# Kernel optimization log

Hardware: AMD Instinct MI355X
Metric: run time of the kernel (lower is better)

Reference implementation:

```python
import jax, jax.numpy as jnp
import numpy as np

B = 32        # graphs per batch
MAXN = 2048   # max nodes per graph (dense batch length)
HEADS = 8
DH = 64       # head dim (512/8)
M = 256       # FAVOR+ random features
D = 512
EPS = 1e-5    # batchnorm eps
KEPS = 1e-6   # performer stabilizer


def _batchnorm(x, g, b):
    # torch BatchNorm1d training-mode: biased batch statistics over node dim
    mu = jnp.mean(x, axis=0)
    var = jnp.mean((x - mu) ** 2, axis=0)
    return (x - mu) * jax.lax.rsqrt(var + EPS) * g + b


def setup_inputs() -> dict:
    key = jax.random.key(0)
    ks = jax.random.split(key, 10)
    sizes = 1024 + (np.arange(B) * 131) % 1025   # ragged graph sizes in [1024, 2048]
    N = int(sizes.sum())                          # 48544
    E = N * 8
    batch = jnp.asarray(np.repeat(np.arange(B), sizes), dtype=jnp.int32)
    edge_index = jax.random.randint(ks[0], (2, E), 0, N, dtype=jnp.int32)
    s = 1.0 / np.sqrt(D)
    return {
        'x': jax.random.normal(ks[1], (N, D), jnp.float32),
        'batch': batch,
        'edge_index': edge_index,
        'norm1_g': jnp.ones((D,), jnp.float32),
        'norm1_b': jnp.zeros((D,), jnp.float32),
        'norm2_g': jnp.ones((D,), jnp.float32),
        'norm2_b': jnp.zeros((D,), jnp.float32),
        'W_conv': jax.random.normal(ks[2], (D, D), jnp.float32) * s,
        'b_conv': jnp.zeros((D,), jnp.float32),
        'Wq': jax.random.normal(ks[3], (D, D), jnp.float32) * s,
        'Wk': jax.random.normal(ks[4], (D, D), jnp.float32) * s,
        'Wv': jax.random.normal(ks[5], (D, D), jnp.float32) * s,
        'Wo': jax.random.normal(ks[6], (D, D), jnp.float32) * s,
        'proj': jax.random.normal(ks[7], (M, DH), jnp.float32),
    }


def _forward(x, batch, edge_index, norm1_g, norm1_b, norm2_g, norm2_b,
             W_conv, b_conv, Wq, Wk, Wv, Wo, proj):
    N = x.shape[0]
    E = edge_index.shape[1]
    h = x

    # norm1 (+ dropout p=0 -> identity) then local GNN conv (mean-agg GCN + linear + relu)
    xn = _batchnorm(x, norm1_g, norm1_b)
    msg = xn[edge_index[0]]                                        # [E, D] gather
    agg = jax.ops.segment_sum(msg, edge_index[1], num_segments=N)  # [N, D] scatter-add
    deg = jax.ops.segment_sum(jnp.ones((E,), x.dtype), edge_index[1], num_segments=N)
    agg = agg / jnp.maximum(deg, 1.0)[:, None]
    conv_out = jax.nn.relu(agg @ W_conv + b_conv)

    # to_dense_batch(h, batch) -> h_dense [B, MAXN, D], mask [B, MAXN]
    counts = jax.ops.segment_sum(jnp.ones((N,), jnp.int32), batch, num_segments=B)
    offsets = jnp.concatenate([jnp.zeros((1,), jnp.int32), jnp.cumsum(counts)[:-1]])
    pos = jnp.arange(N, dtype=jnp.int32) - offsets[batch]
    h_dense = jnp.zeros((B, MAXN, D), x.dtype).at[batch, pos].set(h)
    mask = jnp.zeros((B, MAXN), bool).at[batch, pos].set(True)

    # Performer FAVOR+ non-causal self-attention
    def heads(t, W):
        return (t @ W).reshape(B, MAXN, HEADS, DH).transpose(0, 2, 1, 3)  # [B,H,MAXN,DH]
    q, k, v = heads(h_dense, Wq), heads(h_dense, Wk), heads(h_dense, Wv)

    scale = DH ** -0.25  # data normalizer applied to q and k each

    def phi(t, is_query):
        t = t * scale
        u = jnp.einsum('bhnd,md->bhnm', t, proj)           # [B,H,MAXN,M]
        diag = 0.5 * jnp.sum(t * t, axis=-1, keepdims=True)
        if is_query:
            m_ = jnp.max(u, axis=-1, keepdims=True)
        else:
            m_ = jnp.max(u, axis=(-2, -1), keepdims=True)
        return jnp.exp(u - diag - jax.lax.stop_gradient(m_)) / np.sqrt(M) + KEPS

    qf = phi(q, True)
    kf = phi(k, False) * mask[:, None, :, None]   # zero padded keys
    vm = v * mask[:, None, :, None]

    kv = jnp.einsum('bhnm,bhnd->bhmd', kf, vm)                    # [B,H,M,DH]
    z = 1.0 / (jnp.einsum('bhnm,bhm->bhn', qf, kf.sum(axis=2)) + KEPS)
    attn = jnp.einsum('bhnm,bhmd->bhnd', qf, kv) * z[..., None]   # [B,H,MAXN,DH]
    attn = attn.transpose(0, 2, 1, 3).reshape(B, MAXN, D) @ Wo

    h_attn = attn[batch, pos]                                      # gather back: [mask]

    return _batchnorm(conv_out + h_attn + h, norm2_g, norm2_b)


def reference(x, batch, edge_index, norm1_g, norm1_b, norm2_g, norm2_b,
              W_conv, b_conv, Wq, Wk, Wv, Wo, proj):
    return _forward(x, batch, edge_index, norm1_g, norm1_b, norm2_g, norm2_b,
                    W_conv, b_conv, Wq, Wk, Wv, Wo, proj)
```

## Files before the change

kernel.cpp:

```cpp
#include <hip/hip_runtime.h>
#include <stdint.h>

#define CDIV(a,b) (((a)+(b)-1)/(b))

typedef __attribute__((ext_vector_type(4))) float f32x4;
typedef __attribute__((ext_vector_type(8))) short s16x8;
typedef __attribute__((ext_vector_type(8))) unsigned short u16x8;
typedef __attribute__((ext_vector_type(4))) unsigned short u16x4;

__device__ __forceinline__ float bf2f(unsigned short u) {
  union { unsigned int i; float f; } c; c.i = ((unsigned int)u) << 16; return c.f;
}
__device__ __forceinline__ unsigned short f2bf(float f) {
  union { float f; unsigned int i; } c; c.f = f;
  unsigned int u = c.i;
  u += 0x7fffu + ((u >> 16) & 1u);
  return (unsigned short)(u >> 16);
}

template<int BM, int BN, int WM, int WN, int EPI>
__global__ __launch_bounds__(256) void gemm_bt(
    const unsigned short* __restrict__ A, const unsigned short* __restrict__ B,
    void* __restrict__ Cout, const float* __restrict__ aux,
    int K, int lda, int ldb, int ldc, long zsC, int Mstore)
{
  constexpr int MT = BM / (WM * 16);
  constexpr int NT = BN / (WN * 16);
  constexpr int LDT = 40;
  __shared__ unsigned short As[BM * LDT];
  __shared__ unsigned short Bs[BN * LDT];
  const int tid = threadIdx.x, wid = tid >> 6, lane = tid & 63;
  const int wr = wid / WN, wc = wid % WN;
  long m0 = (long)blockIdx.y * BM;
  const int n0 = blockIdx.x * BN;
  f32x4 acc[MT][NT] = {};
  for (int k0 = 0; k0 < K; k0 += 32) {
    #pragma unroll
    for (int c = tid; c < BM * 4; c += 256) {
      int row = c >> 2, c8 = (c & 3) * 8;
      *(u16x8*)(&As[row * LDT + c8]) = *(const u16x8*)(A + (m0 + row) * lda + k0 + c8);
    }
    #pragma unroll
    for (int c = tid; c < BN * 4; c += 256) {
      int row = c >> 2, c8 = (c & 3) * 8;
      *(u16x8*)(&Bs[row * LDT + c8]) = *(const u16x8*)(B + (long)(n0 + row) * ldb + k0 + c8);
    }
    __syncthreads();
    s16x8 af[MT], bfv[NT];
    #pragma unroll
    for (int mt = 0; mt < MT; mt++)
      af[mt] = *(const s16x8*)(&As[(wr * MT * 16 + mt * 16 + (lane & 15)) * LDT + ((lane >> 4) * 8)]);
    #pragma unroll
    for (int nt = 0; nt < NT; nt++)
      bfv[nt] = *(const s16x8*)(&Bs[(wc * NT * 16 + nt * 16 + (lane & 15)) * LDT + ((lane >> 4) * 8)]);
    #pragma unroll
    for (int mt = 0; mt < MT; mt++)
      #pragma unroll
      for (int nt = 0; nt < NT; nt++)
        acc[mt][nt] = __builtin_amdgcn_mfma_f32_16x16x32_bf16(af[mt], bfv[nt], acc[mt][nt], 0, 0, 0);
    __syncthreads();
  }
  #pragma unroll
  for (int mt = 0; mt < MT; mt++) {
    const int rl0 = wr * (MT * 16) + mt * 16 + ((lane >> 4) << 2);
    #pragma unroll
    for (int nt = 0; nt < NT; nt++) {
      const int col = n0 + wc * (NT * 16) + nt * 16 + (lane & 15);
      #pragma unroll
      for (int i = 0; i < 4; i++) {
        long r = m0 + rl0 + i;
        if (r < Mstore) {
          float v = acc[mt][nt][i];
          long ci = r * ldc + col;
          if constexpr (EPI == 5) {
            float o = v + aux[col];
            o = o > 0.f ? o : 0.f;
            ((float*)Cout)[ci] += o;
          } else if constexpr (EPI == 7) {
            ((unsigned short*)Cout)[(long)(col >> 6) * zsC + r * 64 + (col & 63)] = f2bf(v);
          } else if constexpr (EPI == 8) {
            ((float*)Cout)[ci] = v + aux[ci];
          }
        }
      }
    }
  }
}

__global__ __launch_bounds__(256) void k_kmax(
    const unsigned short* __restrict__ kvqh, const unsigned short* __restrict__ projb,
    const unsigned int* __restrict__ offs, unsigned int* __restrict__ kmax, long Npad) {
  __shared__ float wmax[4];
  const int tid = threadIdx.x, wid = tid >> 6, lane = tid & 63;
  const int b = blockIdx.y, h = blockIdx.z;
  const unsigned int off = offs[b];
  const int nb = (int)(offs[b + 1] - off);
  const int m0 = blockIdx.x * 64;
  if (m0 >= nb) return;
  const unsigned short* A = kvqh + ((long)(8 + h) * Npad + off + m0) * 64;
  f32x4 acc[4][4] = {};
  #pragma unroll
  for (int k0 = 0; k0 < 64; k0 += 32) {
    s16x8 af[4], bfv[4];
    #pragma unroll
    for (int mt = 0; mt < 4; mt++)
      af[mt] = *(const s16x8*)(A + (long)(mt * 16 + (lane & 15)) * 64 + k0 + ((lane >> 4) * 8));
    #pragma unroll
    for (int nt = 0; nt < 4; nt++)
      bfv[nt] = *(const s16x8*)(projb + (long)(wid * 64 + nt * 16 + (lane & 15)) * 64 + k0 + ((lane >> 4) * 8));
    #pragma unroll
    for (int mt = 0; mt < 4; mt++)
      #pragma unroll
      for (int nt = 0; nt < 4; nt++)
        acc[mt][nt] = __builtin_amdgcn_mfma_f32_16x16x32_bf16(af[mt], bfv[nt], acc[mt][nt], 0, 0, 0);
  }
  float bm = -3.0e38f;
  #pragma unroll
  for (int mt = 0; mt < 4; mt++)
    #pragma unroll
    for (int i = 0; i < 4; i++) {
      int row = mt * 16 + ((lane >> 4) << 2) + i;
      if (m0 + row < nb) {
        #pragma unroll
        for (int nt = 0; nt < 4; nt++) bm = fmaxf(bm, acc[mt][nt][i]);
      }
    }
  #pragma unroll
  for (int s = 1; s < 64; s <<= 1) bm = fmaxf(bm, __shfl_xor(bm, s));
  if (lane == 0) wmax[wid] = bm;
  __syncthreads();
  if (tid == 0) {
    float m = fmaxf(fmaxf(wmax[0], wmax[1]), fmaxf(wmax[2], wmax[3]));
    atomicMax(&kmax[b * 8 + h], __float_as_uint(fmaxf(m, 0.f)));
  }
}

__global__ __launch_bounds__(256) void k_kvm(
    const unsigned short* __restrict__ kvqh, const unsigned short* __restrict__ projb,
    const unsigned int* __restrict__ offs, const unsigned int* __restrict__ kmax,
    unsigned short* __restrict__ kvTb, float* __restrict__ kfsum, long Npad) {
  constexpr int TLD = 72;
  __shared__ unsigned short vsT[2][64 * TLD];
  __shared__ unsigned short kfsT[64 * TLD];
  const int tid = threadIdx.x, wid = tid >> 6, lane = tid & 63;
  const int mblk = blockIdx.x, b = blockIdx.y, h = blockIdx.z;
  const unsigned int off = offs[b];
  const int nb = (int)(offs[b + 1] - off);
  const float km = __uint_as_float(kmax[b * 8 + h]);
  const unsigned short* Kp = kvqh + ((long)(8 + h) * Npad + off) * 64;
  const unsigned short* Vp = kvqh + ((long)(16 + h) * Npad + off) * 64;
  const unsigned short* Pp = projb + (long)(mblk * 64 + wid * 16) * 64;
  const int l15 = lane & 15, hi = lane >> 4;
  const int mloc = wid * 16 + l15;

  #pragma unroll
  for (int c = tid; c < 512; c += 256) {
    int row = c >> 3, c8 = (c & 7) * 8;
    int rot = (c & 7) * 8;
    u16x8 v = *(const u16x8*)(Vp + (long)row * 64 + c8);
    #pragma unroll
    for (int j = 0; j < 8; j++) vsT[0][(c8 + j) * TLD + ((row + rot) & 63)] = v[j];
  }
  __syncthreads();

  f32x4 akv[4] = {};
  float ksum = 0.f;
  int buf = 0;
  for (int n0 = 0; n0 < nb; n0 += 64) {
    f32x4 acc[4] = {};
    float dsum[4] = {0.f, 0.f, 0.f, 0.f};
    #pragma unroll
    for (int k0 = 0; k0 < 64; k0 += 32) {
      s16x8 af[4];
      #pragma unroll
      for (int mt = 0; mt < 4; mt++)
        af[mt] = *(const s16x8*)(Kp + ((long)n0 + mt * 16 + l15) * 64 + k0 + hi * 8);
      s16x8 bfv = *(const s16x8*)(Pp + (long)l15 * 64 + k0 + hi * 8);
      #pragma unroll
      for (int mt = 0; mt < 4; mt++) {
        #pragma unroll
        for (int j = 0; j < 8; j++) {
          float a = bf2f((unsigned short)af[mt][j]);
          dsum[mt] += a * a;
        }
        acc[mt] = __builtin_amdgcn_mfma_f32_16x16x32_bf16(af[mt], bfv, acc[mt], 0, 0, 0);
      }
    }
    float rs[4];
    #pragma unroll
    for (int mt = 0; mt < 4; mt++) {
      float s = dsum[mt];
      s += __shfl_xor(s, 16); s += __shfl_xor(s, 32);
      rs[mt] = 0.0625f * s;
    }
    #pragma unroll
    for (int mt = 0; mt < 4; mt++) {
      int r0 = mt * 16 + hi * 4;
      float e[4];
      #pragma unroll
      for (int i = 0; i < 4; i++) {
        float dg = __shfl(rs[mt], hi * 4 + i);
        e[i] = (n0 + r0 + i < nb) ? (__expf(acc[mt][i] - dg - km) * 0.0625f + 1e-6f) : 0.f;
      }
      ksum += e[0] + e[1] + e[2] + e[3];
      unsigned int p0 = (unsigned int)f2bf(e[0]) | ((unsigned int)f2bf(e[1]) << 16);
      unsigned int p1 = (unsigned int)f2bf(e[2]) | ((unsigned int)f2bf(e[3]) << 16);
      *(unsigned int*)(&kfsT[mloc * TLD + r0]) = p0;
      *(unsigned int*)(&kfsT[mloc * TLD + r0 + 2]) = p1;
    }
    if (n0 + 64 < nb) {
      #pragma unroll
      for (int c = tid; c < 512; c += 256) {
        int row = c >> 3, c8 = (c & 7) * 8;
        int rot = (c & 7) * 8;
        u16x8 v = *(const u16x8*)(Vp + ((long)n0 + 64 + row) * 64 + c8);
        #pragma unroll
        for (int j = 0; j < 8; j++) vsT[buf ^ 1][(c8 + j) * TLD + ((row + rot) & 63)] = v[j];
      }
    }
    #pragma unroll
    for (int ks = 0; ks < 2; ks++) {
      s16x8 bB = *(const s16x8*)(&kfsT[mloc * TLD + ks * 32 + hi * 8]);
      #pragma unroll
      for (int mt2 = 0; mt2 < 4; mt2++) {
        int d = mt2 * 16 + l15;
        int rrot = ((ks * 32 + hi * 8) + ((d >> 3) & 7) * 8) & 63;
        s16x8 aA = *(const s16x8*)(&vsT[buf][d * TLD + rrot]);
        akv[mt2] = __builtin_amdgcn_mfma_f32_16x16x32_bf16(aA, bB, akv[mt2], 0, 0, 0);
      }
    }
    __syncthreads();
    buf ^= 1;
  }
  long base = ((long)b * 8 + h) * 16384;
  const int m = mblk * 64 + mloc;
  #pragma unroll
  for (int mt2 = 0; mt2 < 4; mt2++)
    #pragma unroll
    for (int i = 0; i < 4; i++) {
      int d = mt2 * 16 + hi * 4 + i;
      kvTb[base + (long)d * 256 + m] = f2bf(akv[mt2][i]);
    }
  ksum += __shfl_xor(ksum, 16); ksum += __shfl_xor(ksum, 32);
  if (hi == 0) kfsum[((long)b * 8 + h) * 256 + m] = ksum;
}

__global__ __launch_bounds__(256) void k_qflash(
    const unsigned short* __restrict__ qh_all, const unsigned short* __restrict__ projb,
    const unsigned short* __restrict__ kvTb, const float* __restrict__ kfsum,
    const unsigned int* __restrict__ offs, unsigned short* __restrict__ attn, long Npad) {
  constexpr int QLDT = 264;
  __shared__ unsigned short qfs[64 * QLDT];
  __shared__ float skf[256];
  __shared__ float sdiag[64];
  __shared__ float smax[4][64];
  __shared__ float szp[4][64];
  const int tid = threadIdx.x, wid = tid >> 6, lane = tid & 63;
  const int b = blockIdx.y, h = blockIdx.z;
  const unsigned int off = offs[b];
  const int nb = (int)(offs[b + 1] - off);
  const int m0 = blockIdx.x * 64;
  if (m0 >= nb) return;
  const unsigned short* A = qh_all + ((long)h * Npad + off + m0) * 64;
  skf[tid] = kfsum[((long)b * 8 + h) * 256 + tid];
  f32x4 acc[4][4] = {};
  float dsum[4] = {0.f, 0.f, 0.f, 0.f};
  #pragma unroll
  for (int k0 = 0; k0 < 64; k0 += 32) {
    s16x8 af[4], bfv[4];
    #pragma unroll
    for (int mt = 0; mt < 4; mt++)
      af[mt] = *(const s16x8*)(A + (long)(mt * 16 + (lane & 15)) * 64 + k0 + ((lane >> 4) * 8));
    #pragma unroll
    for (int nt = 0; nt < 4; nt++)
      bfv[nt] = *(const s16x8*)(projb + (long)(wid * 64 + nt * 16 + (lane & 15)) * 64 + k0 + ((lane >> 4) * 8));
    if (wid == 0) {
      #pragma unroll
      for (int mt = 0; mt < 4; mt++)
        #pragma unroll
        for (int j = 0; j < 8; j++) {
          float a = bf2f((unsigned short)af[mt][j]);
          dsum[mt] += a * a;
        }
    }
    #pragma unroll
    for (int mt = 0; mt < 4; mt++)
      #pragma unroll
      for (int nt = 0; nt < 4; nt++)
        acc[mt][nt] = __builtin_amdgcn_mfma_f32_16x16x32_bf16(af[mt], bfv[nt], acc[mt][nt], 0, 0, 0);
  }
  if (wid == 0) {
    #pragma unroll
    for (int mt = 0; mt < 4; mt++) {
      float s = dsum[mt];
      s += __shfl_xor(s, 16); s += __shfl_xor(s, 32);
      if (lane < 16) sdiag[mt * 16 + lane] = 0.0625f * s;
    }
  }
  #pragma unroll
  for (int mt = 0; mt < 4; mt++)
    #pragma unroll
    for (int i = 0; i < 4; i++) {
      float rm = fmaxf(fmaxf(acc[mt][0][i], acc[mt][1][i]), fmaxf(acc[mt][2][i], acc[mt][3][i]));
      rm = fmaxf(rm, __shfl_xor(rm, 1)); rm = fmaxf(rm, __shfl_xor(rm, 2));
      rm = fmaxf(rm, __shfl_xor(rm, 4)); rm = fmaxf(rm, __shfl_xor(rm, 8));
      if ((lane & 15) == 0) smax[wid][mt * 16 + ((lane >> 4) << 2) + i] = rm;
    }
  __syncthreads();
  #pragma unroll
  for (int mt = 0; mt < 4; mt++)
    #pragma unroll
    for (int i = 0; i < 4; i++) {
      int row = mt * 16 + ((lane >> 4) << 2) + i;
      float rm = fmaxf(fmaxf(smax[0][row], smax[1][row]), fmaxf(smax[2][row], smax[3][row]));
      float dg = sdiag[row];
      float zp = 0.f;
      #pragma unroll
      for (int nt = 0; nt < 4; nt++) {
        int col = wid * 64 + nt * 16 + (lane & 15);
        float e = __expf(acc[mt][nt][i] - dg - rm) * 0.0625f + 1e-6f;
        qfs[row * QLDT + col] = f2bf(e);
        zp += e * skf[col];
      }
      zp += __shfl_xor(zp, 1); zp += __shfl_xor(zp, 2);
      zp += __shfl_xor(zp, 4); zp += __shfl_xor(zp, 8);
      if ((lane & 15) == 0) szp[wid][row] = zp;
    }
  __syncthreads();
  const unsigned short* kvb = kvTb + ((long)b * 8 + h) * 16384;
  f32x4 acc2[4] = {};
  #pragma unroll
  for (int ks = 0; ks < 8; ks++) {
    s16x8 aq = *(const s16x8*)(&qfs[(wid * 16 + (lane & 15)) * QLDT + ks * 32 + ((lane >> 4) * 8)]);
    #pragma unroll
    for (int ntd = 0; ntd < 4; ntd++) {
      s16x8 bk = *(const s16x8*)(kvb + (long)(ntd * 16 + (lane & 15)) * 256 + ks * 32 + ((lane >> 4) * 8));
      acc2[ntd] = __builtin_amdgcn_mfma_f32_16x16x32_bf16(aq, bk, acc2[ntd], 0, 0, 0);
    }
  }
  #pragma unroll
  for (int ntd = 0; ntd < 4; ntd++)
    #pragma unroll
    for (int i = 0; i < 4; i++) {
      int row = wid * 16 + ((lane >> 4) << 2) + i;
      if (m0 + row < nb) {
        float zr = 1.f / (szp[0][row] + szp[1][row] + szp[2][row] + szp[3][row] + 1e-6f);
        attn[(long)(off + m0 + row) * 512 + h * 64 + ntd * 16 + (lane & 15)] = f2bf(acc2[ntd][i] * zr);
      }
    }
}


__global__ void k_fill(float* __restrict__ out, long n, float v) {
  long i = (long)blockIdx.x * 256 + threadIdx.x;
  if (i < n) out[i] = v;
}

__global__ void k_convert_x(const float* __restrict__ x, unsigned short* __restrict__ xb,
                            long ntotal, long nreal) {
  long i = ((long)blockIdx.x * 256 + threadIdx.x) * 4;
  if (i >= ntotal) return;
  u16x4 o;
  if (i < nreal) {
    f32x4 v = *(const f32x4*)(x + i);
    o[0] = f2bf(v[0]); o[1] = f2bf(v[1]); o[2] = f2bf(v[2]); o[3] = f2bf(v[3]);
  } else { o[0] = 0; o[1] = 0; o[2] = 0; o[3] = 0; }
  *(u16x4*)(xb + i) = o;
}

__global__ void k_transall(const float* __restrict__ w0, const float* __restrict__ w1,
                           const float* __restrict__ w2, const float* __restrict__ w3,
                           const float* __restrict__ w4, unsigned short* __restrict__ out) {
  long idx = (long)blockIdx.x * 256 + threadIdx.x;
  if (idx >= (5L << 18)) return;
  int which = (int)(idx >> 18);
  int r = (int)(idx & 262143);
  int n = r >> 9, k = r & 511;
  const float* w = which == 0 ? w0 : which == 1 ? w1 : which == 2 ? w2 : which == 3 ? w3 : w4;
  out[idx] = f2bf(w[k * 512 + n]);
}

__global__ void k_scale_copy_bf(const float* __restrict__ in, unsigned short* __restrict__ out,
                                int n, float scl) {
  int i = blockIdx.x * 256 + threadIdx.x;
  if (i < n) out[i] = f2bf(in[i] * scl);
}

__global__ void k_bn_stats(const float* __restrict__ x, float* __restrict__ s1,
                           float* __restrict__ s2, int N, int rpb) {
  int t = threadIdx.x;
  int r0 = blockIdx.x * rpb;
  int r1 = min(N, r0 + rpb);
  float a1 = 0, a2 = 0, b1 = 0, b2 = 0;
  for (int r = r0; r < r1; r++) {
    float va = x[(long)r * 512 + t];
    float vb = x[(long)r * 512 + t + 256];
    a1 += va; a2 += va * va; b1 += vb; b2 += vb * vb;
  }
  atomicAdd(&s1[t], a1); atomicAdd(&s2[t], a2);
  atomicAdd(&s1[t + 256], b1); atomicAdd(&s2[t + 256], b2);
}

__global__ void k_bn_final(const float* __restrict__ s1, const float* __restrict__ s2,
                           const float* __restrict__ g, const float* __restrict__ b,
                           float* __restrict__ a, float* __restrict__ c, float invN) {
  int t = threadIdx.x;
  float mu = s1[t] * invN;
  float var = s2[t] * invN - mu * mu;
  float inv = rsqrtf(var + 1e-5f);
  float av = g[t] * inv;
  a[t] = av;
  c[t] = b[t] - mu * av;
}

__global__ void k_deg(const int* __restrict__ ed, unsigned int* __restrict__ deg, long E) {
  long i = (long)blockIdx.x * 256 + threadIdx.x;
  if (i < E) atomicAdd(&deg[ed[i]], 1u);
}

__global__ void k_offs(const int* __restrict__ batch, unsigned int* __restrict__ offs, int N) {
  int i = blockIdx.x * 256 + threadIdx.x;
  if (i >= N) return;
  int b = batch[i];
  if (i == 0) { for (int bb = 0; bb <= b; bb++) offs[bb] = 0; }
  else {
    int pb = batch[i - 1];
    if (pb != b) for (int bb = pb + 1; bb <= b; bb++) offs[bb] = i;
  }
  if (i == N - 1) { for (int bb = b + 1; bb <= 32; bb++) offs[bb] = N; }
}

__global__ __launch_bounds__(1024) void k_scan_nodes(const unsigned int* __restrict__ deg,
                                                     unsigned int* __restrict__ rowstart, int N) {
  __shared__ unsigned int wsum[16];
  __shared__ unsigned int carry_s;
  int t = threadIdx.x, lane = t & 63, wid = t >> 6;
  if (t == 0) carry_s = 0;
  __syncthreads();
  for (int base = 0; base < N; base += 1024) {
    int i = base + t;
    unsigned int v = (i < N) ? deg[i] : 0;
    unsigned int sc = v;
    #pragma unroll
    for (int s = 1; s < 64; s <<= 1) {
      unsigned int u = __shfl_up(sc, s);
      if (lane >= s) sc += u;
    }
    if (lane == 63) wsum[wid] = sc;
    __syncthreads();
    unsigned int woff = 0, tot = 0;
    #pragma unroll
    for (int w = 0; w < 16; w++) { unsigned int s = wsum[w]; if (w < wid) woff += s; tot += s; }
    unsigned int carry = carry_s;
    if (i < N) rowstart[i] = carry + woff + sc - v;
    __syncthreads();
    if (t == 0) carry_s = carry + tot;
    __syncthreads();
  }
  if (threadIdx.x == 0) rowstart[N] = carry_s;
}

__global__ void k_csr_fill(const int* __restrict__ es, const int* __restrict__ ed,
                           const unsigned int* __restrict__ rowstart,
                           unsigned int* __restrict__ cursor, int* __restrict__ csr, long E) {
  long e = (long)blockIdx.x * 256 + threadIdx.x;
  if (e >= E) return;
  int d = ed[e];
  unsigned int slot = atomicAdd(&cursor[d], 1u);
  csr[rowstart[d] + slot] = es[e];
}

__global__ __launch_bounds__(128) void k_gather(const int* __restrict__ csr,
                                                const unsigned int* __restrict__ rowstart,
                                                const float* __restrict__ x,
                                                const float* __restrict__ a1, const float* __restrict__ c1,
                                                unsigned short* __restrict__ conv_in, int N) {
  long n = blockIdx.x;
  int c = threadIdx.x * 4;
  u16x4 o; o[0] = 0; o[1] = 0; o[2] = 0; o[3] = 0;
  if (n < N) {
    unsigned int r0 = rowstart[n], r1 = rowstart[n + 1];
    if (r1 > r0) {
      f32x4 acc0 = {}, acc1 = {};
      unsigned int j = r0;
      for (; j + 2 <= r1; j += 2) {
        int s0 = csr[j], s1 = csr[j + 1];
        acc0 += *(const f32x4*)(x + (long)s0 * 512 + c);
        acc1 += *(const f32x4*)(x + (long)s1 * 512 + c);
      }
      if (j < r1) { int s0 = csr[j]; acc0 += *(const f32x4*)(x + (long)s0 * 512 + c); }
      f32x4 acc = acc0 + acc1;
      float inv = 1.f / (float)(r1 - r0);
      o[0] = f2bf(acc[0] * inv * a1[c + 0] + c1[c + 0]);
      o[1] = f2bf(acc[1] * inv * a1[c + 1] + c1[c + 1]);
      o[2] = f2bf(acc[2] * inv * a1[c + 2] + c1[c + 2]);
      o[3] = f2bf(acc[3] * inv * a1[c + 3] + c1[c + 3]);
    }
  }
  *(u16x4*)(conv_in + n * 512 + c) = o;
}

__global__ void k_stats(const float* __restrict__ y, float* __restrict__ s1,
                        float* __restrict__ s2, int N, int rpb) {
  int t = threadIdx.x;
  int r0 = blockIdx.x * rpb;
  int r1 = min(N, r0 + rpb);
  float a1 = 0, a2 = 0, b1 = 0, b2 = 0;
  for (int r = r0; r < r1; r++) {
    float va = y[(long)r * 512 + t];
    float vb = y[(long)r * 512 + t + 256];
    a1 += va; a2 += va * va; b1 += vb; b2 += vb * vb;
  }
  atomicAdd(&s1[t], a1); atomicAdd(&s2[t], a2);
  atomicAdd(&s1[t + 256], b1); atomicAdd(&s2[t + 256], b2);
}

__global__ void k_bn_apply(float* __restrict__ y, const float* __restrict__ a,
                           const float* __restrict__ c, long total) {
  long i4 = ((long)blockIdx.x * 256 + threadIdx.x) * 4;
  if (i4 >= total) return;
  int col = (int)(i4 & 511);
  f32x4 v = *(const f32x4*)(y + i4);
  #pragma unroll
  for (int j = 0; j < 4; j++) v[j] = v[j] * a[col + j] + c[col + j];
  *(f32x4*)(y + i4) = v;
}


extern "C" void kernel_launch(void* const* d_in, const int* in_sizes, int n_in,
                              void* d_out, int out_size, void* d_ws, size_t ws_size,
                              hipStream_t stream) {
  (void)n_in; (void)out_size;
  const float* x = (const float*)d_in[0];
  const int* batch = (const int*)d_in[1];
  const int* eidx = (const int*)d_in[2];
  const float* n1g = (const float*)d_in[3];
  const float* n1b = (const float*)d_in[4];
  const float* n2g = (const float*)d_in[5];
  const float* n2b = (const float*)d_in[6];
  const float* wconv = (const float*)d_in[7];
  const float* bconv = (const float*)d_in[8];
  const float* wq = (const float*)d_in[9];
  const float* wk = (const float*)d_in[10];
  const float* wv = (const float*)d_in[11];
  const float* wo = (const float*)d_in[12];
  const float* proj = (const float*)d_in[13];

  const int N = in_sizes[1];
  const long E = in_sizes[2] / 2;
  const long Npad = CDIV(N, 128) * 128 + 256;
  const int Mb = (int)((CDIV(N, 128) * 128 + 128) / 128);
  const int* es = eidx;
  const int* ed = eidx + E;
  float* out = (float*)d_out;

  char* p = (char*)d_ws;
  auto alloc = [&](size_t bytes) -> char* {
    char* r = p;
    p += (bytes + 255) & ~(size_t)255;
    return r;
  };
  unsigned short* kvqh = (unsigned short*)alloc((size_t)24 * Npad * 64 * 2);
  unsigned short* xbf  = (unsigned short*)alloc((size_t)Npad * 512 * 2);
  unsigned short* kvT_b = (unsigned short*)alloc((size_t)32 * 8 * 16384 * 2);
  unsigned short* wts   = (unsigned short*)alloc((size_t)5 * 512 * 512 * 2);
  unsigned short* proj_s = (unsigned short*)alloc((size_t)256 * 64 * 2);
  float* bn1_acc = (float*)alloc(1024 * 4);
  float* bn1_ac  = (float*)alloc(1024 * 4);
  float* bn2_acc = (float*)alloc(1024 * 4);
  float* bn2_ac  = (float*)alloc(1024 * 4);
  unsigned int* deg      = (unsigned int*)alloc((size_t)N * 4);
  unsigned int* offs     = (unsigned int*)alloc(33 * 4);
  unsigned int* kmax     = (unsigned int*)alloc(32 * 8 * 4);
  float* kfsum = (float*)alloc((size_t)32 * 8 * 256 * 4);
  unsigned int* rowstart = (unsigned int*)alloc((size_t)(N + 1) * 4);
  unsigned int* cursor   = (unsigned int*)alloc((size_t)N * 4);
  int* csr               = (int*)alloc((size_t)E * 4);
  size_t required = (size_t)(p - (char*)d_ws);
  if (required > ws_size) {
    k_fill<<<(int)CDIV((long)N * 512, 256), 256, 0, stream>>>(
        out, (long)N * 512, 1.0e6f + (float)(ws_size >> 20));
    return;
  }
  unsigned short* wqkv_t  = wts;
  unsigned short* wconv_t = wts + 3 * 512 * 512;
  unsigned short* wo_t    = wts + 4 * 512 * 512;
  unsigned short* attn_all = xbf;
  unsigned short* conv_in  = xbf;

  hipMemsetAsync(deg, 0, (size_t)N * 4, stream);
  hipMemsetAsync(cursor, 0, (size_t)N * 4, stream);
  hipMemsetAsync(kmax, 0, 32 * 8 * 4, stream);
  hipMemsetAsync(bn1_acc, 0, 1024 * 4, stream);
  hipMemsetAsync(bn2_acc, 0, 1024 * 4, stream);

  k_convert_x<<<(int)CDIV(Npad * 512 / 4, 256), 256, 0, stream>>>(x, xbf, Npad * 512, (long)N * 512);
  k_transall<<<(int)CDIV(5L << 18, 256), 256, 0, stream>>>(wq, wk, wv, wconv, wo, wts);
  k_scale_copy_bf<<<CDIV(256 * 64, 256), 256, 0, stream>>>(proj, proj_s, 256 * 64, 0.35355339059327373f);

  int rpb = CDIV(N, 1024);
  k_bn_stats<<<1024, 256, 0, stream>>>(x, bn1_acc, bn1_acc + 512, N, rpb);
  k_bn_final<<<1, 512, 0, stream>>>(bn1_acc, bn1_acc + 512, n1g, n1b, bn1_ac, bn1_ac + 512, 1.f / N);
  k_deg<<<(int)CDIV(E, 256), 256, 0, stream>>>(ed, deg, E);
  k_offs<<<CDIV(N, 256), 256, 0, stream>>>(batch, offs, N);
  k_scan_nodes<<<1, 1024, 0, stream>>>(deg, rowstart, N);
  k_csr_fill<<<(int)CDIV(E, 256), 256, 0, stream>>>(es, ed, rowstart, cursor, csr, E);

  gemm_bt<128, 128, 2, 2, 7><<<dim3(12, Mb), 256, 0, stream>>>(
      xbf, wqkv_t, kvqh, nullptr, 512, 512, 512, 0, (long)Npad * 64, (int)Npad);

  k_kmax<<<dim3(32, 32, 8), 256, 0, stream>>>(kvqh, proj_s, offs, kmax, Npad);
  k_kvm<<<dim3(4, 32, 8), 256, 0, stream>>>(kvqh, proj_s, offs, kmax, kvT_b, kfsum, Npad);

  k_qflash<<<dim3(32, 32, 8), 256, 0, stream>>>(
      kvqh, proj_s, kvT_b, kfsum, offs, attn_all, Npad);

  gemm_bt<128, 128, 2, 2, 8><<<dim3(4, Mb), 256, 0, stream>>>(
      attn_all, wo_t, out, x, 512, 512, 512, 512, 0, N);

  k_gather<<<(int)(CDIV(N, 128) * 128), 128, 0, stream>>>(csr, rowstart, x, bn1_ac, bn1_ac + 512, conv_in, N);
  gemm_bt<128, 128, 2, 2, 5><<<dim3(4, Mb), 256, 0, stream>>>(
      conv_in, wconv_t, out, bconv, 512, 512, 512, 512, 0, N);

  k_stats<<<1024, 256, 0, stream>>>(out, bn2_acc, bn2_acc + 512, N, rpb);
  k_bn_final<<<1, 512, 0, stream>>>(bn2_acc, bn2_acc + 512, n2g, n2b, bn2_ac, bn2_ac + 512, 1.f / N);
  k_bn_apply<<<(int)CDIV((long)N * 512 / 4, 256), 256, 0, stream>>>(out, bn2_ac, bn2_ac + 512, (long)N * 512);
}
```

Before: 1.187 ms.

## Restructure query feature kernel per-wave and fold normalizer into kv matmul

```diff
diff --git a/kernel.cpp b/kernel.cpp
--- a/kernel.cpp
+++ b/kernel.cpp
@@ -17,6 +17,8 @@
   u += 0x7fffu + ((u >> 16) & 1u);
   return (unsigned short)(u >> 16);
 }
+
+#define KVROWS 80
 
 template<int BM, int BN, int WM, int WN, int EPI>
 __global__ __launch_bounds__(256) void gemm_bt(
@@ -138,7 +140,7 @@
 __global__ __launch_bounds__(256) void k_kvm(
     const unsigned short* __restrict__ kvqh, const unsigned short* __restrict__ projb,
     const unsigned int* __restrict__ offs, const unsigned int* __restrict__ kmax,
-    unsigned short* __restrict__ kvTb, float* __restrict__ kfsum, long Npad) {
+    unsigned short* __restrict__ kvTb, long Npad) {
   constexpr int TLD = 72;
   __shared__ unsigned short vsT[2][64 * TLD];
   __shared__ unsigned short kfsT[64 * TLD];
@@ -232,7 +234,7 @@
     __syncthreads();
     buf ^= 1;
   }
-  long base = ((long)b * 8 + h) * 16384;
+  long base = ((long)b * 8 + h) * (KVROWS * 256);
   const int m = mblk * 64 + mloc;
   #pragma unroll
   for (int mt2 = 0; mt2 < 4; mt2++)
@@ -242,112 +244,82 @@
       kvTb[base + (long)d * 256 + m] = f2bf(akv[mt2][i]);
     }
   ksum += __shfl_xor(ksum, 16); ksum += __shfl_xor(ksum, 32);
-  if (hi == 0) kfsum[((long)b * 8 + h) * 256 + m] = ksum;
-}
-
-__global__ __launch_bounds__(256) void k_qflash(
+  if (hi == 0) kvTb[base + 64 * 256 + m] = f2bf(ksum);
+}
+
+__global__ __launch_bounds__(256, 4) void k_qflash(
     const unsigned short* __restrict__ qh_all, const unsigned short* __restrict__ projb,
-    const unsigned short* __restrict__ kvTb, const float* __restrict__ kfsum,
-    const unsigned int* __restrict__ offs, unsigned short* __restrict__ attn, long Npad) {
+    const unsigned short* __restrict__ kvTb, const unsigned int* __restrict__ offs,
+    unsigned short* __restrict__ attn, long Npad) {
   constexpr int QLDT = 264;
-  __shared__ unsigned short qfs[64 * QLDT];
-  __shared__ float skf[256];
-  __shared__ float sdiag[64];
-  __shared__ float smax[4][64];
-  __shared__ float szp[4][64];
+  __shared__ unsigned short qfs[4][16 * QLDT];
   const int tid = threadIdx.x, wid = tid >> 6, lane = tid & 63;
+  const int l15 = lane & 15, hi = lane >> 4;
   const int b = blockIdx.y, h = blockIdx.z;
   const unsigned int off = offs[b];
   const int nb = (int)(offs[b + 1] - off);
-  const int m0 = blockIdx.x * 64;
+  const int m0 = blockIdx.x * 64 + wid * 16;
   if (m0 >= nb) return;
-  const unsigned short* A = qh_all + ((long)h * Npad + off + m0) * 64;
-  skf[tid] = kfsum[((long)b * 8 + h) * 256 + tid];
-  f32x4 acc[4][4] = {};
-  float dsum[4] = {0.f, 0.f, 0.f, 0.f};
+  const unsigned short* Q = qh_all + ((long)h * Npad + off + m0) * 64;
+
+  f32x4 acc[16] = {};
+  float dsq = 0.f;
   #pragma unroll
   for (int k0 = 0; k0 < 64; k0 += 32) {
-    s16x8 af[4], bfv[4];
-    #pragma unroll
-    for (int mt = 0; mt < 4; mt++)
-      af[mt] = *(const s16x8*)(A + (long)(mt * 16 + (lane & 15)) * 64 + k0 + ((lane >> 4) * 8));
-    #pragma unroll
-    for (int nt = 0; nt < 4; nt++)
-      bfv[nt] = *(const s16x8*)(projb + (long)(wid * 64 + nt * 16 + (lane & 15)) * 64 + k0 + ((lane >> 4) * 8));
-    if (wid == 0) {
-      #pragma unroll
-      for (int mt = 0; mt < 4; mt++)
-        #pragma unroll
-        for (int j = 0; j < 8; j++) {
-          float a = bf2f((unsigned short)af[mt][j]);
-          dsum[mt] += a * a;
-        }
-    }
-    #pragma unroll
-    for (int mt = 0; mt < 4; mt++)
-      #pragma unroll
-      for (int nt = 0; nt < 4; nt++)
-        acc[mt][nt] = __builtin_amdgcn_mfma_f32_16x16x32_bf16(af[mt], bfv[nt], acc[mt][nt], 0, 0, 0);
-  }
-  if (wid == 0) {
-    #pragma unroll
-    for (int mt = 0; mt < 4; mt++) {
-      float s = dsum[mt];
-      s += __shfl_xor(s, 16); s += __shfl_xor(s, 32);
-      if (lane < 16) sdiag[mt * 16 + lane] = 0.0625f * s;
-    }
-  }
-  #pragma unroll
-  for (int mt = 0; mt < 4; mt++)
-    #pragma unroll
-    for (int i = 0; i < 4; i++) {
-      float rm = fmaxf(fmaxf(acc[mt][0][i], acc[mt][1][i]), fmaxf(acc[mt][2][i], acc[mt][3][i]));
-      rm = fmaxf(rm, __shfl_xor(rm, 1)); rm = fmaxf(rm, __shfl_xor(rm, 2));
-      rm = fmaxf(rm, __shfl_xor(rm, 4)); rm = fmaxf(rm, __shfl_xor(rm, 8));
-      if ((lane & 15) == 0) smax[wid][mt * 16 + ((lane >> 4) << 2) + i] = rm;
-    }
-  __syncthreads();
-  #pragma unroll
-  for (int mt = 0; mt < 4; mt++)
-    #pragma unroll
-    for (int i = 0; i < 4; i++) {
-      int row = mt * 16 + ((lane >> 4) << 2) + i;
-      float rm = fmaxf(fmaxf(smax[0][row], smax[1][row]), fmaxf(smax[2][row], smax[3][row]));
-      float dg = sdiag[row];
-      float zp = 0.f;
-      #pragma unroll
-      for (int nt = 0; nt < 4; nt++) {
-        int col = wid * 64 + nt * 16 + (lane & 15);
-        float e = __expf(acc[mt][nt][i] - dg - rm) * 0.0625f + 1e-6f;
-        qfs[row * QLDT + col] = f2bf(e);
-        zp += e * skf[col];
-      }
-      zp += __shfl_xor(zp, 1); zp += __shfl_xor(zp, 2);
-      zp += __shfl_xor(zp, 4); zp += __shfl_xor(zp, 8);
-      if ((lane & 15) == 0) szp[wid][row] = zp;
-    }
-  __syncthreads();
-  const unsigned short* kvb = kvTb + ((long)b * 8 + h) * 16384;
-  f32x4 acc2[4] = {};
+    s16x8 bfv = *(const s16x8*)(Q + (long)l15 * 64 + k0 + hi * 8);
+    #pragma unroll
+    for (int j = 0; j < 8; j++) {
+      float qv = bf2f((unsigned short)bfv[j]);
+      dsq += qv * qv;
+    }
+    #pragma unroll
+    for (int mt = 0; mt < 16; mt++) {
+      s16x8 af = *(const s16x8*)(projb + (long)(mt * 16 + l15) * 64 + k0 + hi * 8);
+      acc[mt] = __builtin_amdgcn_mfma_f32_16x16x32_bf16(af, bfv, acc[mt], 0, 0, 0);
+    }
+  }
+  dsq += __shfl_xor(dsq, 16); dsq += __shfl_xor(dsq, 32);
+  float rm = -3.0e38f;
+  #pragma unroll
+  for (int mt = 0; mt < 16; mt++)
+    #pragma unroll
+    for (int i = 0; i < 4; i++) rm = fmaxf(rm, acc[mt][i]);
+  rm = fmaxf(rm, __shfl_xor(rm, 16)); rm = fmaxf(rm, __shfl_xor(rm, 32));
+  const float sub = 0.0625f * dsq + rm;
+
+  unsigned short* myq = &qfs[wid][0];
+  #pragma unroll
+  for (int mt = 0; mt < 16; mt++) {
+    u16x4 o;
+    #pragma unroll
+    for (int i = 0; i < 4; i++)
+      o[i] = f2bf(__expf(acc[mt][i] - sub) * 0.0625f + 1e-6f);
+    *(u16x4*)(&myq[l15 * QLDT + mt * 16 + hi * 4]) = o;
+  }
+
+  const unsigned short* kvb = kvTb + ((long)b * 8 + h) * (KVROWS * 256);
+  f32x4 acc2[5] = {};
   #pragma unroll
   for (int ks = 0; ks < 8; ks++) {
-    s16x8 aq = *(const s16x8*)(&qfs[(wid * 16 + (lane & 15)) * QLDT + ks * 32 + ((lane >> 4) * 8)]);
-    #pragma unroll
-    for (int ntd = 0; ntd < 4; ntd++) {
-      s16x8 bk = *(const s16x8*)(kvb + (long)(ntd * 16 + (lane & 15)) * 256 + ks * 32 + ((lane >> 4) * 8));
-      acc2[ntd] = __builtin_amdgcn_mfma_f32_16x16x32_bf16(aq, bk, acc2[ntd], 0, 0, 0);
-    }
-  }
-  #pragma unroll
-  for (int ntd = 0; ntd < 4; ntd++)
-    #pragma unroll
-    for (int i = 0; i < 4; i++) {
-      int row = wid * 16 + ((lane >> 4) << 2) + i;
-      if (m0 + row < nb) {
-        float zr = 1.f / (szp[0][row] + szp[1][row] + szp[2][row] + szp[3][row] + 1e-6f);
-        attn[(long)(off + m0 + row) * 512 + h * 64 + ntd * 16 + (lane & 15)] = f2bf(acc2[ntd][i] * zr);
-      }
-    }
+    s16x8 bq = *(const s16x8*)(&myq[l15 * QLDT + ks * 32 + hi * 8]);
+    #pragma unroll
+    for (int t = 0; t < 5; t++) {
+      s16x8 ak = *(const s16x8*)(kvb + (long)(t * 16 + l15) * 256 + ks * 32 + hi * 8);
+      acc2[t] = __builtin_amdgcn_mfma_f32_16x16x32_bf16(ak, bq, acc2[t], 0, 0, 0);
+    }
+  }
+  float zden = __shfl(acc2[4][0], l15);
+  float zr = 1.f / (zden + 1e-6f);
+  if (m0 + l15 < nb) {
+    unsigned short* po = attn + (long)(off + m0 + l15) * 512 + h * 64;
+    #pragma unroll
+    for (int t = 0; t < 4; t++) {
+      u16x4 o;
+      #pragma unroll
+      for (int i = 0; i < 4; i++) o[i] = f2bf(acc2[t][i] * zr);
+      *(u16x4*)(po + t * 16 + hi * 4) = o;
+    }
+  }
 }
 
 
@@ -356,16 +328,21 @@
   if (i < n) out[i] = v;
 }
 
-__global__ void k_convert_x(const float* __restrict__ x, unsigned short* __restrict__ xb,
-                            long ntotal, long nreal) {
-  long i = ((long)blockIdx.x * 256 + threadIdx.x) * 4;
-  if (i >= ntotal) return;
-  u16x4 o;
-  if (i < nreal) {
-    f32x4 v = *(const f32x4*)(x + i);
-    o[0] = f2bf(v[0]); o[1] = f2bf(v[1]); o[2] = f2bf(v[2]); o[3] = f2bf(v[3]);
-  } else { o[0] = 0; o[1] = 0; o[2] = 0; o[3] = 0; }
-  *(u16x4*)(xb + i) = o;
+__global__ void k_convx_stats(const float* __restrict__ x, unsigned short* __restrict__ xb,
+                              float* __restrict__ s1, float* __restrict__ s2, int N, int rpb) {
+  int t = threadIdx.x;
+  int r0 = blockIdx.x * rpb;
+  int r1 = min(N, r0 + rpb);
+  float a1 = 0, a2 = 0, b1 = 0, b2 = 0;
+  for (int r = r0; r < r1; r++) {
+    const float* xr = x + (long)r * 512 + 2 * t;
+    float va = xr[0], vb = xr[1];
+    a1 += va; a2 += va * va; b1 += vb; b2 += vb * vb;
+    *(unsigned int*)(xb + (long)r * 512 + 2 * t) =
+        (unsigned int)f2bf(va) | ((unsigned int)f2bf(vb) << 16);
+  }
+  atomicAdd(&s1[2 * t], a1); atomicAdd(&s2[2 * t], a2);
+  atomicAdd(&s1[2 * t + 1], b1); atomicAdd(&s2[2 * t + 1], b2);
 }
 
 __global__ void k_transall(const float* __restrict__ w0, const float* __restrict__ w1,
@@ -384,21 +361,6 @@
                                 int n, float scl) {
   int i = blockIdx.x * 256 + threadIdx.x;
   if (i < n) out[i] = f2bf(in[i] * scl);
-}
-
-__global__ void k_bn_stats(const float* __restrict__ x, float* __restrict__ s1,
-                           float* __restrict__ s2, int N, int rpb) {
-  int t = threadIdx.x;
-  int r0 = blockIdx.x * rpb;
-  int r1 = min(N, r0 + rpb);
-  float a1 = 0, a2 = 0, b1 = 0, b2 = 0;
-  for (int r = r0; r < r1; r++) {
-    float va = x[(long)r * 512 + t];
-    float vb = x[(long)r * 512 + t + 256];
-    a1 += va; a2 += va * va; b1 += vb; b2 += vb * vb;
-  }
-  atomicAdd(&s1[t], a1); atomicAdd(&s2[t], a2);
-  atomicAdd(&s1[t + 256], b1); atomicAdd(&s2[t + 256], b2);
 }
 
 __global__ void k_bn_final(const float* __restrict__ s1, const float* __restrict__ s2,
@@ -562,7 +524,7 @@
   };
   unsigned short* kvqh = (unsigned short*)alloc((size_t)24 * Npad * 64 * 2);
   unsigned short* xbf  = (unsigned short*)alloc((size_t)Npad * 512 * 2);
-  unsigned short* kvT_b = (unsigned short*)alloc((size_t)32 * 8 * 16384 * 2);
+  unsigned short* kvT_b = (unsigned short*)alloc((size_t)32 * 8 * KVROWS * 256 * 2);
   unsigned short* wts   = (unsigned short*)alloc((size_t)5 * 512 * 512 * 2);
   unsigned short* proj_s = (unsigned short*)alloc((size_t)256 * 64 * 2);
   float* bn1_acc = (float*)alloc(1024 * 4);
@@ -572,7 +534,6 @@
   unsigned int* deg      = (unsigned int*)alloc((size_t)N * 4);
   unsigned int* offs     = (unsigned int*)alloc(33 * 4);
   unsigned int* kmax     = (unsigned int*)alloc(32 * 8 * 4);
-  float* kfsum = (float*)alloc((size_t)32 * 8 * 256 * 4);
   unsigned int* rowstart = (unsigned int*)alloc((size_t)(N + 1) * 4);
   unsigned int* cursor   = (unsigned int*)alloc((size_t)N * 4);
   int* csr               = (int*)alloc((size_t)E * 4);
@@ -593,13 +554,13 @@
   hipMemsetAsync(kmax, 0, 32 * 8 * 4, stream);
   hipMemsetAsync(bn1_acc, 0, 1024 * 4, stream);
   hipMemsetAsync(bn2_acc, 0, 1024 * 4, stream);
-
-  k_convert_x<<<(int)CDIV(Npad * 512 / 4, 256), 256, 0, stream>>>(x, xbf, Npad * 512, (long)N * 512);
+  hipMemsetAsync(kvT_b, 0, (size_t)32 * 8 * KVROWS * 256 * 2, stream);
+  hipMemsetAsync(xbf + (size_t)N * 512, 0, (size_t)(Npad - N) * 512 * 2, stream);
+
+  int rpb = CDIV(N, 1024);
+  k_convx_stats<<<1024, 256, 0, stream>>>(x, xbf, bn1_acc, bn1_acc + 512, N, rpb);
   k_transall<<<(int)CDIV(5L << 18, 256), 256, 0, stream>>>(wq, wk, wv, wconv, wo, wts);
   k_scale_copy_bf<<<CDIV(256 * 64, 256), 256, 0, stream>>>(proj, proj_s, 256 * 64, 0.35355339059327373f);
-
-  int rpb = CDIV(N, 1024);
-  k_bn_stats<<<1024, 256, 0, stream>>>(x, bn1_acc, bn1_acc + 512, N, rpb);
   k_bn_final<<<1, 512, 0, stream>>>(bn1_acc, bn1_acc + 512, n1g, n1b, bn1_ac, bn1_ac + 512, 1.f / N);
   k_deg<<<(int)CDIV(E, 256), 256, 0, stream>>>(ed, deg, E);
   k_offs<<<CDIV(N, 256), 256, 0, stream>>>(batch, offs, N);
@@ -610,10 +571,10 @@
       xbf, wqkv_t, kvqh, nullptr, 512, 512, 512, 0, (long)Npad * 64, (int)Npad);
 
   k_kmax<<<dim3(32, 32, 8), 256, 0, stream>>>(kvqh, proj_s, offs, kmax, Npad);
-  k_kvm<<<dim3(4, 32, 8), 256, 0, stream>>>(kvqh, proj_s, offs, kmax, kvT_b, kfsum, Npad);
+  k_kvm<<<dim3(4, 32, 8), 256, 0, stream>>>(kvqh, proj_s, offs, kmax, kvT_b, Npad);
 
   k_qflash<<<dim3(32, 32, 8), 256, 0, stream>>>(
-      kvqh, proj_s, kvT_b, kfsum, offs, attn_all, Npad);
+      kvqh, proj_s, kvT_b, offs, attn_all, Npad);
 
   gemm_bt<128, 128, 2, 2, 8><<<dim3(4, Mb), 256, 0, stream>>>(
       attn_all, wo_t, out, x, 512, 512, 512, 512, 0, N);
```

Measured after the change: 1.259 ms. 1.06x slower.
